# Optimization experiments

Measured on AMD Instinct MI355X. Metric: run time of the kernel, lower is better.

## Reference

```python
import jax, jax.numpy as jnp
import numpy as np

B, S, I, H, O = 64, 1024, 512, 1024, 512

def setup_inputs() -> dict:
    key = jax.random.key(0)
    ks = jax.random.split(key, 4)
    scale_ih = float(np.sqrt(6.0 / (I + H)))
    scale_hh = float(np.sqrt(6.0 / (H + H)))
    scale_ho = float(np.sqrt(6.0 / (H + O)))
    return {
        "inputs": jax.random.normal(ks[0], (B, S, I), dtype=jnp.float32),
        "initial_hidden": jnp.zeros((B, H), dtype=jnp.float32),
        "W_ih": jax.random.uniform(ks[1], (H, I), jnp.float32, -scale_ih, scale_ih),
        "b_ih": jnp.zeros((H,), jnp.float32),
        "W_hh": jax.random.uniform(ks[2], (H, H), jnp.float32, -scale_hh, scale_hh),
        "b_hh": jnp.zeros((H,), jnp.float32),
        "W_ho": jax.random.uniform(ks[3], (O, H), jnp.float32, -scale_ho, scale_ho),
        "b_ho": jnp.zeros((O,), jnp.float32),
    }

def reference(inputs, initial_hidden, W_ih, b_ih, W_hh, b_hh, W_ho, b_ho):
    # h_t = tanh(W_ih x_t + b_ih + W_hh h_{t-1} + b_hh); y_t = W_ho h_t + b_ho
    # Precompute the input projection for all timesteps in one batched GEMM.
    x_proj = jnp.einsum("bsi,hi->bsh", inputs, W_ih) + b_ih + b_hh  # (B,S,H)

    def step(h, xp_t):
        h_new = jnp.tanh(xp_t + h @ W_hh.T)  # (B,H)
        return h_new, h_new

    # scan over time: move seq axis to front
    last_hidden, hs = jax.lax.scan(step, initial_hidden, jnp.swapaxes(x_proj, 0, 1))
    hs = jnp.swapaxes(hs, 0, 1)  # (B,S,H)
    outputs = jnp.einsum("bsh,oh->bso", hs, W_ho) + b_ho  # (B,S,O)
    return outputs, last_hidden
```

## Files before the change

### kernel.cpp

```cpp
#include <hip/hip_runtime.h>
#include <cmath>

#define B_ 64
#define S_ 1024
#define I_ 512
#define H_ 1024
#define O_ 512
#define HB (H_ * B_)
#define SCAN_NBLK 64
#define PROD_NBLK 96
#define WORK_NBLK 96
#define NTHR 512
#define NPROD_PER_S 8
#define SPIN_BUDGET (1 << 22)

typedef __attribute__((ext_vector_type(8))) __bf16 bf16x8;
typedef __attribute__((ext_vector_type(4))) float f32x4;
typedef unsigned long long u64;

__device__ __forceinline__ int fragIdx(int k, int b) {
  int kt = k >> 5, q = (k >> 3) & 3, slot = k & 7;
  int nt = b >> 4, ln = q * 16 + (b & 15);
  return (((kt * 4 + nt) * 64) + ln) * 8 + slot;
}

__device__ __forceinline__ float aload_f32(const float* p) {
  unsigned v = __hip_atomic_load((const unsigned*)p, __ATOMIC_RELAXED,
                                 __HIP_MEMORY_SCOPE_AGENT);
  return __builtin_bit_cast(float, v);
}

__global__ void k_hfrag0(const float* __restrict__ h0,
                         unsigned short* __restrict__ hh,
                         unsigned short* __restrict__ hl) {
  int idx = blockIdx.x * 256 + threadIdx.x;
  int b = idx >> 10, k = idx & 1023;
  float v = h0[(size_t)b * H_ + k];
  __bf16 h = (__bf16)v;
  __bf16 l = (__bf16)(v - (float)h);
  int fi = fragIdx(k, b);
  hh[fi] = __builtin_bit_cast(unsigned short, h);
  hl[fi] = __builtin_bit_cast(unsigned short, l);
}

__global__ __launch_bounds__(NTHR) void k_fused(
    const float* __restrict__ Whh, float* __restrict__ xp,
    unsigned short* __restrict__ hh0, unsigned short* __restrict__ hl0,
    unsigned short* __restrict__ hh1, unsigned short* __restrict__ hl1,
    unsigned* __restrict__ bar,
    const float* __restrict__ Who, const float* __restrict__ bho,
    float* __restrict__ out,
    const float* __restrict__ x, const float* __restrict__ Wih,
    const float* __restrict__ bih, const float* __restrict__ bhh) {
  __shared__ float sh[9216];
  const int t = threadIdx.x;
  unsigned* dn    = bar + 128;
  unsigned* incnt = bar + 256;
  int budget = SPIN_BUDGET;

  if (blockIdx.x < SCAN_NBLK) {
    float* red  = sh;
    float* hbuf = sh + 8192;
    const int lane = t & 63;
    const int w    = t >> 6;
    const int j0   = blockIdx.x * 16;
    const int m    = lane & 15, q = lane >> 4;

    bf16x8 Ahi[4], Alo[4];
    #pragma unroll
    for (int kta = 0; kta < 4; kta++) {
      const float* src = Whh + (size_t)(j0 + m) * H_ + (w * 128 + kta * 32 + q * 8);
      float4 v0 = *(const float4*)src;
      float4 v1 = *(const float4*)(src + 4);
      float vv[8] = {v0.x, v0.y, v0.z, v0.w, v1.x, v1.y, v1.z, v1.w};
      #pragma unroll
      for (int j = 0; j < 8; j++) {
        __bf16 h = (__bf16)vv[j];
        __bf16 l = (__bf16)(vv[j] - (float)h);
        Ahi[kta][j] = h;
        Alo[kta][j] = l;
      }
    }

    const int jA = t >> 6, bA = t & 63;
    const size_t xi0 = (size_t)(j0 + jA) * 64 + bA;
    const size_t xi1 = (size_t)(j0 + 8 + jA) * 64 + bA;

    while (__hip_atomic_load(&incnt[0], __ATOMIC_RELAXED,
                             __HIP_MEMORY_SCOPE_AGENT) < NPROD_PER_S) {
      if (--budget < 0) break;
      __builtin_amdgcn_s_sleep(16);
    }
    float xc0 = aload_f32(&xp[xi0]);
    float xc1 = aload_f32(&xp[xi1]);

    const unsigned short* rdh = hh0;
    const unsigned short* rdl = hl0;
    unsigned short* wrh = hh1;
    unsigned short* wrl = hl1;

    for (int s = 0; s < S_; s++) {
      f32x4 acc0 = 0.f, acc1 = 0.f, acc2 = 0.f, acc3 = 0.f;
      #pragma unroll
      for (int kta = 0; kta < 4; kta++) {
        const int ktg = w * 4 + kta;
        const unsigned short* ph = rdh + ((size_t)(ktg * 4) * 64 + lane) * 8;
        const unsigned short* pl = rdl + ((size_t)(ktg * 4) * 64 + lane) * 8;
        bf16x8 bh0 = __builtin_bit_cast(bf16x8, *(const uint4*)(ph + 0 * 512));
        bf16x8 bh1 = __builtin_bit_cast(bf16x8, *(const uint4*)(ph + 1 * 512));
        bf16x8 bh2 = __builtin_bit_cast(bf16x8, *(const uint4*)(ph + 2 * 512));
        bf16x8 bh3 = __builtin_bit_cast(bf16x8, *(const uint4*)(ph + 3 * 512));
        bf16x8 bl0 = __builtin_bit_cast(bf16x8, *(const uint4*)(pl + 0 * 512));
        bf16x8 bl1 = __builtin_bit_cast(bf16x8, *(const uint4*)(pl + 1 * 512));
        bf16x8 bl2 = __builtin_bit_cast(bf16x8, *(const uint4*)(pl + 2 * 512));
        bf16x8 bl3 = __builtin_bit_cast(bf16x8, *(const uint4*)(pl + 3 * 512));
        acc0 = __builtin_amdgcn_mfma_f32_16x16x32_bf16(Ahi[kta], bh0, acc0, 0, 0, 0);
        acc1 = __builtin_amdgcn_mfma_f32_16x16x32_bf16(Ahi[kta], bh1, acc1, 0, 0, 0);
        acc2 = __builtin_amdgcn_mfma_f32_16x16x32_bf16(Ahi[kta], bh2, acc2, 0, 0, 0);
        acc3 = __builtin_amdgcn_mfma_f32_16x16x32_bf16(Ahi[kta], bh3, acc3, 0, 0, 0);
        acc0 = __builtin_amdgcn_mfma_f32_16x16x32_bf16(Alo[kta], bh0, acc0, 0, 0, 0);
        acc1 = __builtin_amdgcn_mfma_f32_16x16x32_bf16(Alo[kta], bh1, acc1, 0, 0, 0);
        acc2 = __builtin_amdgcn_mfma_f32_16x16x32_bf16(Alo[kta], bh2, acc2, 0, 0, 0);
        acc3 = __builtin_amdgcn_mfma_f32_16x16x32_bf16(Alo[kta], bh3, acc3, 0, 0, 0);
        acc0 = __builtin_amdgcn_mfma_f32_16x16x32_bf16(Ahi[kta], bl0, acc0, 0, 0, 0);
        acc1 = __builtin_amdgcn_mfma_f32_16x16x32_bf16(Ahi[kta], bl1, acc1, 0, 0, 0);
        acc2 = __builtin_amdgcn_mfma_f32_16x16x32_bf16(Ahi[kta], bl2, acc2, 0, 0, 0);
        acc3 = __builtin_amdgcn_mfma_f32_16x16x32_bf16(Ahi[kta], bl3, acc3, 0, 0, 0);
      }
      *(f32x4*)&red[(((w * 4 + 0) * 64) + lane) * 4] = acc0;
      *(f32x4*)&red[(((w * 4 + 1) * 64) + lane) * 4] = acc1;
      *(f32x4*)&red[(((w * 4 + 2) * 64) + lane) * 4] = acc2;
      *(f32x4*)&red[(((w * 4 + 3) * 64) + lane) * 4] = acc3;
      __syncthreads();
      float* hcur = xp + (size_t)s * HB;
      #pragma unroll
      for (int rep = 0; rep < 2; rep++) {
        const int j = jA + rep * 8, b = bA;
        const int nt = b >> 4, lc = (j >> 2) * 16 + (b & 15), reg = j & 3;
        float sum = 0.f;
        #pragma unroll
        for (int ww = 0; ww < 8; ww++)
          sum += red[(((ww * 4 + nt) * 64) + lc) * 4 + reg];
        const size_t xi = (rep == 0) ? xi0 : xi1;
        const float xv = (rep == 0) ? xc0 : xc1;
        float v = tanhf(xv + sum);
        __hip_atomic_store(&hcur[xi], v, __ATOMIC_RELAXED, __HIP_MEMORY_SCOPE_AGENT);
        hbuf[j * 64 + b] = v;
      }
      __syncthreads();
      if (t < 128) {
        const int jg = t >> 6, b = t & 63;
        const int k0 = j0 + jg * 8;
        const int kt = k0 >> 5, qq = (k0 >> 3) & 3;
        const int nt = b >> 4, ln = qq * 16 + (b & 15);
        const size_t fb = ((size_t)((kt * 4 + nt) * 64 + ln)) * 8;
        unsigned hu[8], lu[8];
        #pragma unroll
        for (int jj = 0; jj < 8; jj++) {
          float v = hbuf[(jg * 8 + jj) * 64 + b];
          __bf16 hh = (__bf16)v;
          __bf16 ll = (__bf16)(v - (float)hh);
          hu[jj] = (unsigned)__builtin_bit_cast(unsigned short, hh);
          lu[jj] = (unsigned)__builtin_bit_cast(unsigned short, ll);
        }
        u64 hw0 = (u64)hu[0] | ((u64)hu[1] << 16) | ((u64)hu[2] << 32) | ((u64)hu[3] << 48);
        u64 hw1 = (u64)hu[4] | ((u64)hu[5] << 16) | ((u64)hu[6] << 32) | ((u64)hu[7] << 48);
        u64 lw0 = (u64)lu[0] | ((u64)lu[1] << 16) | ((u64)lu[2] << 32) | ((u64)lu[3] << 48);
        u64 lw1 = (u64)lu[4] | ((u64)lu[5] << 16) | ((u64)lu[6] << 32) | ((u64)lu[7] << 48);
        __hip_atomic_store((u64*)(wrh + fb) + 0, hw0, __ATOMIC_RELAXED, __HIP_MEMORY_SCOPE_AGENT);
        __hip_atomic_store((u64*)(wrh + fb) + 1, hw1, __ATOMIC_RELAXED, __HIP_MEMORY_SCOPE_AGENT);
        __hip_atomic_store((u64*)(wrl + fb) + 0, lw0, __ATOMIC_RELAXED, __HIP_MEMORY_SCOPE_AGENT);
        __hip_atomic_store((u64*)(wrl + fb) + 1, lw1, __ATOMIC_RELAXED, __HIP_MEMORY_SCOPE_AGENT);
      }
      __syncthreads();
      if (t == 0)
        __hip_atomic_store(&bar[blockIdx.x], (unsigned)(s + 1),
                           __ATOMIC_RELAXED, __HIP_MEMORY_SCOPE_AGENT);
      const int sn = s + 1;
      const float* xpn = xp + (size_t)sn * HB;
      if (t >= 64) {
        if (sn < S_) {
          while (__hip_atomic_load(&incnt[sn], __ATOMIC_RELAXED,
                                   __HIP_MEMORY_SCOPE_AGENT) < NPROD_PER_S) {
            if (--budget < 0) break;
            __builtin_amdgcn_s_sleep(1);
          }
          xc0 = aload_f32(&xpn[xi0]); xc1 = aload_f32(&xpn[xi1]);
        }
      } else {
        __builtin_amdgcn_fence(__ATOMIC_ACQUIRE, "agent");
        if (sn < S_) {
          while (__hip_atomic_load(&incnt[sn], __ATOMIC_RELAXED,
                                   __HIP_MEMORY_SCOPE_AGENT) < NPROD_PER_S) {
            if (--budget < 0) break;
            __builtin_amdgcn_s_sleep(1);
          }
          xc0 = aload_f32(&xpn[xi0]); xc1 = aload_f32(&xpn[xi1]);
        }
        const unsigned need = (unsigned)sn;
        while (__hip_atomic_load(&bar[lane], __ATOMIC_RELAXED,
                                 __HIP_MEMORY_SCOPE_AGENT) < need) {
          if (--budget < 0) break;
          __builtin_amdgcn_s_sleep(1);
        }
        if (t == 0 && blockIdx.x == 0)
          __hip_atomic_store(dn, (unsigned)sn,
                             __ATOMIC_RELAXED, __HIP_MEMORY_SCOPE_AGENT);
      }
      __syncthreads();
      const unsigned short* th = rdh; rdh = wrh; wrh = (unsigned short*)th;
      const unsigned short* tl = rdl; rdl = wrl; wrl = (unsigned short*)tl;
    }
  } else if (blockIdx.x < SCAN_NBLK + PROD_NBLK) {
    float* As = sh;
    float* Bs = sh + 128 * 36;
    const int pid = blockIdx.x - SCAN_NBLK;
    const int tx = t & 15, ty = t >> 4;
    const int bS = t >> 3, c4S = (t & 7) * 4;
    for (int item = pid; item < S_ * 8; item += PROD_NBLK) {
      const int s = item >> 3, h00 = (item & 7) << 7;
      float acc[4][4] = {};
      for (int k0 = 0; k0 < I_; k0 += 32) {
        #pragma unroll
        for (int L = 0; L < 2; L++) {
          int f = L * 512 + t;
          int row = f >> 3, c4 = (f & 7) * 4;
          float4 v = *(const float4*)&Wih[(size_t)(h00 + row) * I_ + k0 + c4];
          *(float4*)&As[row * 36 + c4] = v;
        }
        {
          float4 v = *(const float4*)&x[(size_t)bS * (S_ * I_) + (size_t)s * I_ + k0 + c4S];
          Bs[(c4S + 0) * 72 + bS] = v.x;
          Bs[(c4S + 1) * 72 + bS] = v.y;
          Bs[(c4S + 2) * 72 + bS] = v.z;
          Bs[(c4S + 3) * 72 + bS] = v.w;
        }
        __syncthreads();
        #pragma unroll
        for (int k = 0; k < 32; k += 4) {
          float4 a[4], bq[4];
          #pragma unroll
          for (int r = 0; r < 4; r++) a[r] = *(const float4*)&As[(ty * 4 + r) * 36 + k];
          #pragma unroll
          for (int kk = 0; kk < 4; kk++) bq[kk] = *(const float4*)&Bs[(k + kk) * 72 + tx * 4];
          #pragma unroll
          for (int kk = 0; kk < 4; kk++)
            #pragma unroll
            for (int r = 0; r < 4; r++)
              #pragma unroll
              for (int c = 0; c < 4; c++)
                acc[r][c] += ((const float*)&a[r])[kk] * ((const float*)&bq[kk])[c];
        }
        __syncthreads();
      }
      #pragma unroll
      for (int r = 0; r < 4; r++) {
        const int h = h00 + ty * 4 + r;
        const float bias = bih[h] + bhh[h];
        float2 p0 = {acc[r][0] + bias, acc[r][1] + bias};
        float2 p1 = {acc[r][2] + bias, acc[r][3] + bias};
        u64* dst = (u64*)&xp[(size_t)s * HB + (size_t)h * 64 + tx * 4];
        __hip_atomic_store(dst + 0, __builtin_bit_cast(u64, p0),
                           __ATOMIC_RELAXED, __HIP_MEMORY_SCOPE_AGENT);
        __hip_atomic_store(dst + 1, __builtin_bit_cast(u64, p1),
                           __ATOMIC_RELAXED, __HIP_MEMORY_SCOPE_AGENT);
      }
      __syncthreads();
      if (t == 0)
        __hip_atomic_fetch_add(&incnt[s], 1u,
                               __ATOMIC_RELAXED, __HIP_MEMORY_SCOPE_AGENT);
    }
  } else {
    float* As = sh;
    float* Bs = sh + 32 * 68;
    const int wid = blockIdx.x - SCAN_NBLK - PROD_NBLK;
    const int tx = t & 31, ty = t >> 5;
    const int kkA = t >> 4, b4 = (t & 15) * 4;
    for (int item = wid; item < S_ * 4; item += WORK_NBLK) {
      const int s = item >> 2, o0 = (item & 3) << 7;
      if (t == 0) {
        const unsigned need = (unsigned)(s + 1);
        while (__hip_atomic_load(dn, __ATOMIC_RELAXED,
                                 __HIP_MEMORY_SCOPE_AGENT) < need) {
          if (--budget < 0) break;
          __builtin_amdgcn_s_sleep(8);
        }
      }
      __syncthreads();
      const float* hsS = xp + (size_t)s * HB;
      float acc[4][4] = {};
      for (int k0 = 0; k0 < H_; k0 += 32) {
        const u64* hp = (const u64*)&hsS[(size_t)(k0 + kkA) * 64 + b4];
        u64 w0 = __hip_atomic_load(hp + 0, __ATOMIC_RELAXED, __HIP_MEMORY_SCOPE_AGENT);
        u64 w1 = __hip_atomic_load(hp + 1, __ATOMIC_RELAXED, __HIP_MEMORY_SCOPE_AGENT);
        *(float2*)&As[kkA * 68 + b4 + 0] = __builtin_bit_cast(float2, w0);
        *(float2*)&As[kkA * 68 + b4 + 2] = __builtin_bit_cast(float2, w1);
        #pragma unroll
        for (int L = 0; L < 2; L++) {
          int f = L * 512 + t;
          int row = f >> 3, c4 = (f & 7) * 4;
          float4 v = *(const float4*)&Who[(size_t)(o0 + row) * H_ + k0 + c4];
          Bs[(c4 + 0) * 132 + row] = v.x;
          Bs[(c4 + 1) * 132 + row] = v.y;
          Bs[(c4 + 2) * 132 + row] = v.z;
          Bs[(c4 + 3) * 132 + row] = v.w;
        }
        __syncthreads();
        #pragma unroll
        for (int k = 0; k < 32; k++) {
          float4 a4 = *(const float4*)&As[k * 68 + ty * 4];
          float4 bq = *(const float4*)&Bs[k * 132 + tx * 4];
          #pragma unroll
          for (int r = 0; r < 4; r++)
            #pragma unroll
            for (int c = 0; c < 4; c++)
              acc[r][c] += ((const float*)&a4)[r] * ((const float*)&bq)[c];
        }
        __syncthreads();
      }
      #pragma unroll
      for (int r = 0; r < 4; r++) {
        const int b = ty * 4 + r;
        float4 o4;
        o4.x = acc[r][0] + bho[o0 + tx * 4 + 0];
        o4.y = acc[r][1] + bho[o0 + tx * 4 + 1];
        o4.z = acc[r][2] + bho[o0 + tx * 4 + 2];
        o4.w = acc[r][3] + bho[o0 + tx * 4 + 3];
        *(float4*)&out[(size_t)b * (S_ * O_) + (size_t)s * O_ + o0 + tx * 4] = o4;
      }
    }
  }
}

__global__ void k_lasth(const float* __restrict__ hlast, float* __restrict__ out) {
  int idx = blockIdx.x * 256 + threadIdx.x;
  int b = idx >> 10, h = idx & 1023;
  out[idx] = hlast[h * 64 + b];
}

extern "C" void kernel_launch(void* const* d_in, const int* in_sizes, int n_in,
                              void* d_out, int out_size, void* d_ws, size_t ws_size,
                              hipStream_t stream) {
  const float* x    = (const float*)d_in[0];
  const float* h0   = (const float*)d_in[1];
  const float* Wih  = (const float*)d_in[2];
  const float* bih  = (const float*)d_in[3];
  const float* Whh  = (const float*)d_in[4];
  const float* bhh  = (const float*)d_in[5];
  const float* Who  = (const float*)d_in[6];
  const float* bho  = (const float*)d_in[7];
  float* out = (float*)d_out;

  float* xp = (float*)d_ws;
  unsigned short* hh0 = (unsigned short*)(xp + (size_t)S_ * HB);
  unsigned short* hl0 = hh0 + HB;
  unsigned short* hh1 = hl0 + HB;
  unsigned short* hl1 = hh1 + HB;
  unsigned* bar = (unsigned*)(hl1 + HB);

  hipMemsetAsync(bar, 0, 8192, stream);
  k_hfrag0<<<256, 256, 0, stream>>>(h0, hh0, hl0);

  void* args[] = {(void*)&Whh, (void*)&xp, (void*)&hh0, (void*)&hl0,
                  (void*)&hh1, (void*)&hl1, (void*)&bar,
                  (void*)&Who, (void*)&bho, (void*)&out,
                  (void*)&x, (void*)&Wih, (void*)&bih, (void*)&bhh};
  hipLaunchCooperativeKernel((const void*)k_fused,
                             dim3(SCAN_NBLK + PROD_NBLK + WORK_NBLK), dim3(NTHR),
                             args, 0, stream);

  k_lasth<<<256, 256, 0, stream>>>(xp + (size_t)(S_ - 1) * HB, out + (size_t)B_ * S_ * O_);
}
```

Measured before the change: 6.426 ms.

## Halve scan blocks to 32, each computing 32 hidden rows, and add producer blocks

Each recurrent-scan block now owns 32 rows of W_hh (two 16-row MFMA tiles) rather than 16. That halves the number of blocks in the per-step grid barrier, and the freed CUs go to the input-projection producer and output worker roles. The xp prefetch now uses plain loads after a compiler memory barrier instead of atomic loads, and the spin budget and sleep interval are reduced. The risks are double the MFMA work per block on the serial critical path, extra register pressure from twice as many A fragments, and correctness that depends on plain loads seeing values other blocks just wrote.

New measurement: 6.196 ms. -3.6%, faster.

```diff
diff --git a/kernel.cpp b/kernel.cpp
--- a/kernel.cpp
+++ b/kernel.cpp
@@ -7,12 +7,12 @@
 #define H_ 1024
 #define O_ 512
 #define HB (H_ * B_)
-#define SCAN_NBLK 64
-#define PROD_NBLK 96
-#define WORK_NBLK 96
+#define SCAN_NBLK 32
+#define PROD_NBLK 112
+#define WORK_NBLK 112
 #define NTHR 512
 #define NPROD_PER_S 8
-#define SPIN_BUDGET (1 << 22)
+#define SPIN_BUDGET (1 << 20)
 
 typedef __attribute__((ext_vector_type(8))) __bf16 bf16x8;
 typedef __attribute__((ext_vector_type(4))) float f32x4;
@@ -22,12 +22,6 @@
   int kt = k >> 5, q = (k >> 3) & 3, slot = k & 7;
   int nt = b >> 4, ln = q * 16 + (b & 15);
   return (((kt * 4 + nt) * 64) + ln) * 8 + slot;
-}
-
-__device__ __forceinline__ float aload_f32(const float* p) {
-  unsigned v = __hip_atomic_load((const unsigned*)p, __ATOMIC_RELAXED,
-                                 __HIP_MEMORY_SCOPE_AGENT);
-  return __builtin_bit_cast(float, v);
 }
 
 __global__ void k_hfrag0(const float* __restrict__ h0,
@@ -52,7 +46,7 @@
     float* __restrict__ out,
     const float* __restrict__ x, const float* __restrict__ Wih,
     const float* __restrict__ bih, const float* __restrict__ bhh) {
-  __shared__ float sh[9216];
+  __shared__ float sh[10240];
   const int t = threadIdx.x;
   unsigned* dn    = bar + 128;
   unsigned* incnt = bar + 256;
@@ -63,36 +57,45 @@
     float* hbuf = sh + 8192;
     const int lane = t & 63;
     const int w    = t >> 6;
-    const int j0   = blockIdx.x * 16;
+    const int j0   = blockIdx.x * 32;
     const int m    = lane & 15, q = lane >> 4;
 
-    bf16x8 Ahi[4], Alo[4];
+    bf16x8 Ahi[2][4], Alo[2][4];
     #pragma unroll
-    for (int kta = 0; kta < 4; kta++) {
-      const float* src = Whh + (size_t)(j0 + m) * H_ + (w * 128 + kta * 32 + q * 8);
-      float4 v0 = *(const float4*)src;
-      float4 v1 = *(const float4*)(src + 4);
-      float vv[8] = {v0.x, v0.y, v0.z, v0.w, v1.x, v1.y, v1.z, v1.w};
-      #pragma unroll
-      for (int j = 0; j < 8; j++) {
-        __bf16 h = (__bf16)vv[j];
-        __bf16 l = (__bf16)(vv[j] - (float)h);
-        Ahi[kta][j] = h;
-        Alo[kta][j] = l;
-      }
-    }
+    for (int mt = 0; mt < 2; mt++)
+      #pragma unroll
+      for (int kta = 0; kta < 4; kta++) {
+        const float* src = Whh + (size_t)(j0 + mt * 16 + m) * H_ +
+                           (w * 128 + kta * 32 + q * 8);
+        float4 v0 = *(const float4*)src;
+        float4 v1 = *(const float4*)(src + 4);
+        float vv[8] = {v0.x, v0.y, v0.z, v0.w, v1.x, v1.y, v1.z, v1.w};
+        #pragma unroll
+        for (int j = 0; j < 8; j++) {
+          __bf16 h = (__bf16)vv[j];
+          __bf16 l = (__bf16)(vv[j] - (float)h);
+          Ahi[mt][kta][j] = h;
+          Alo[mt][kta][j] = l;
+        }
+      }
 
     const int jA = t >> 6, bA = t & 63;
-    const size_t xi0 = (size_t)(j0 + jA) * 64 + bA;
-    const size_t xi1 = (size_t)(j0 + 8 + jA) * 64 + bA;
+    size_t xia[4];
+    #pragma unroll
+    for (int mt = 0; mt < 2; mt++)
+      #pragma unroll
+      for (int rep = 0; rep < 2; rep++)
+        xia[mt * 2 + rep] = (size_t)(j0 + mt * 16 + jA + rep * 8) * 64 + bA;
 
     while (__hip_atomic_load(&incnt[0], __ATOMIC_RELAXED,
                              __HIP_MEMORY_SCOPE_AGENT) < NPROD_PER_S) {
       if (--budget < 0) break;
-      __builtin_amdgcn_s_sleep(16);
+      __builtin_amdgcn_s_sleep(8);
     }
-    float xc0 = aload_f32(&xp[xi0]);
-    float xc1 = aload_f32(&xp[xi1]);
+    asm volatile("" ::: "memory");
+    float xc[4];
+    #pragma unroll
+    for (int p = 0; p < 4; p++) xc[p] = xp[xia[p]];
 
     const unsigned short* rdh = hh0;
     const unsigned short* rdl = hl0;
@@ -100,7 +103,11 @@
     unsigned short* wrl = hl1;
 
     for (int s = 0; s < S_; s++) {
-      f32x4 acc0 = 0.f, acc1 = 0.f, acc2 = 0.f, acc3 = 0.f;
+      f32x4 acc[2][4];
+      #pragma unroll
+      for (int mt = 0; mt < 2; mt++)
+        #pragma unroll
+        for (int i = 0; i < 4; i++) acc[mt][i] = 0.f;
       #pragma unroll
       for (int kta = 0; kta < 4; kta++) {
         const int ktg = w * 4 + kta;
@@ -114,41 +121,45 @@
         bf16x8 bl1 = __builtin_bit_cast(bf16x8, *(const uint4*)(pl + 1 * 512));
         bf16x8 bl2 = __builtin_bit_cast(bf16x8, *(const uint4*)(pl + 2 * 512));
         bf16x8 bl3 = __builtin_bit_cast(bf16x8, *(const uint4*)(pl + 3 * 512));
-        acc0 = __builtin_amdgcn_mfma_f32_16x16x32_bf16(Ahi[kta], bh0, acc0, 0, 0, 0);
-        acc1 = __builtin_amdgcn_mfma_f32_16x16x32_bf16(Ahi[kta], bh1, acc1, 0, 0, 0);
-        acc2 = __builtin_amdgcn_mfma_f32_16x16x32_bf16(Ahi[kta], bh2, acc2, 0, 0, 0);
-        acc3 = __builtin_amdgcn_mfma_f32_16x16x32_bf16(Ahi[kta], bh3, acc3, 0, 0, 0);
-        acc0 = __builtin_amdgcn_mfma_f32_16x16x32_bf16(Alo[kta], bh0, acc0, 0, 0, 0);
-        acc1 = __builtin_amdgcn_mfma_f32_16x16x32_bf16(Alo[kta], bh1, acc1, 0, 0, 0);
-        acc2 = __builtin_amdgcn_mfma_f32_16x16x32_bf16(Alo[kta], bh2, acc2, 0, 0, 0);
-        acc3 = __builtin_amdgcn_mfma_f32_16x16x32_bf16(Alo[kta], bh3, acc3, 0, 0, 0);
-        acc0 = __builtin_amdgcn_mfma_f32_16x16x32_bf16(Ahi[kta], bl0, acc0, 0, 0, 0);
-        acc1 = __builtin_amdgcn_mfma_f32_16x16x32_bf16(Ahi[kta], bl1, acc1, 0, 0, 0);
-        acc2 = __builtin_amdgcn_mfma_f32_16x16x32_bf16(Ahi[kta], bl2, acc2, 0, 0, 0);
-        acc3 = __builtin_amdgcn_mfma_f32_16x16x32_bf16(Ahi[kta], bl3, acc3, 0, 0, 0);
-      }
-      *(f32x4*)&red[(((w * 4 + 0) * 64) + lane) * 4] = acc0;
-      *(f32x4*)&red[(((w * 4 + 1) * 64) + lane) * 4] = acc1;
-      *(f32x4*)&red[(((w * 4 + 2) * 64) + lane) * 4] = acc2;
-      *(f32x4*)&red[(((w * 4 + 3) * 64) + lane) * 4] = acc3;
-      __syncthreads();
+        #pragma unroll
+        for (int mt = 0; mt < 2; mt++) {
+          acc[mt][0] = __builtin_amdgcn_mfma_f32_16x16x32_bf16(Ahi[mt][kta], bh0, acc[mt][0], 0, 0, 0);
+          acc[mt][1] = __builtin_amdgcn_mfma_f32_16x16x32_bf16(Ahi[mt][kta], bh1, acc[mt][1], 0, 0, 0);
+          acc[mt][2] = __builtin_amdgcn_mfma_f32_16x16x32_bf16(Ahi[mt][kta], bh2, acc[mt][2], 0, 0, 0);
+          acc[mt][3] = __builtin_amdgcn_mfma_f32_16x16x32_bf16(Ahi[mt][kta], bh3, acc[mt][3], 0, 0, 0);
+          acc[mt][0] = __builtin_amdgcn_mfma_f32_16x16x32_bf16(Alo[mt][kta], bh0, acc[mt][0], 0, 0, 0);
+          acc[mt][1] = __builtin_amdgcn_mfma_f32_16x16x32_bf16(Alo[mt][kta], bh1, acc[mt][1], 0, 0, 0);
+          acc[mt][2] = __builtin_amdgcn_mfma_f32_16x16x32_bf16(Alo[mt][kta], bh2, acc[mt][2], 0, 0, 0);
+          acc[mt][3] = __builtin_amdgcn_mfma_f32_16x16x32_bf16(Alo[mt][kta], bh3, acc[mt][3], 0, 0, 0);
+          acc[mt][0] = __builtin_amdgcn_mfma_f32_16x16x32_bf16(Ahi[mt][kta], bl0, acc[mt][0], 0, 0, 0);
+          acc[mt][1] = __builtin_amdgcn_mfma_f32_16x16x32_bf16(Ahi[mt][kta], bl1, acc[mt][1], 0, 0, 0);
+          acc[mt][2] = __builtin_amdgcn_mfma_f32_16x16x32_bf16(Ahi[mt][kta], bl2, acc[mt][2], 0, 0, 0);
+          acc[mt][3] = __builtin_amdgcn_mfma_f32_16x16x32_bf16(Ahi[mt][kta], bl3, acc[mt][3], 0, 0, 0);
+        }
+      }
       float* hcur = xp + (size_t)s * HB;
       #pragma unroll
-      for (int rep = 0; rep < 2; rep++) {
-        const int j = jA + rep * 8, b = bA;
-        const int nt = b >> 4, lc = (j >> 2) * 16 + (b & 15), reg = j & 3;
-        float sum = 0.f;
-        #pragma unroll
-        for (int ww = 0; ww < 8; ww++)
-          sum += red[(((ww * 4 + nt) * 64) + lc) * 4 + reg];
-        const size_t xi = (rep == 0) ? xi0 : xi1;
-        const float xv = (rep == 0) ? xc0 : xc1;
-        float v = tanhf(xv + sum);
-        __hip_atomic_store(&hcur[xi], v, __ATOMIC_RELAXED, __HIP_MEMORY_SCOPE_AGENT);
-        hbuf[j * 64 + b] = v;
-      }
-      __syncthreads();
-      if (t < 128) {
+      for (int mt = 0; mt < 2; mt++) {
+        #pragma unroll
+        for (int i = 0; i < 4; i++)
+          *(f32x4*)&red[(((w * 4 + i) * 64) + lane) * 4] = acc[mt][i];
+        __syncthreads();
+        #pragma unroll
+        for (int rep = 0; rep < 2; rep++) {
+          const int j = jA + rep * 8, b = bA;
+          const int nt = b >> 4, lc = (j >> 2) * 16 + (b & 15), reg = j & 3;
+          float sum = 0.f;
+          #pragma unroll
+          for (int ww = 0; ww < 8; ww++)
+            sum += red[(((ww * 4 + nt) * 64) + lc) * 4 + reg];
+          float v = tanhf(xc[mt * 2 + rep] + sum);
+          __hip_atomic_store(&hcur[xia[mt * 2 + rep]], v,
+                             __ATOMIC_RELAXED, __HIP_MEMORY_SCOPE_AGENT);
+          hbuf[(mt * 16 + j) * 64 + b] = v;
+        }
+        __syncthreads();
+      }
+      if (t < 256) {
         const int jg = t >> 6, b = t & 63;
         const int k0 = j0 + jg * 8;
         const int kt = k0 >> 5, qq = (k0 >> 3) & 3;
@@ -185,7 +196,9 @@
             if (--budget < 0) break;
             __builtin_amdgcn_s_sleep(1);
           }
-          xc0 = aload_f32(&xpn[xi0]); xc1 = aload_f32(&xpn[xi1]);
+          asm volatile("" ::: "memory");
+          #pragma unroll
+          for (int p = 0; p < 4; p++) xc[p] = xpn[xia[p]];
         }
       } else {
         __builtin_amdgcn_fence(__ATOMIC_ACQUIRE, "agent");
@@ -195,13 +208,17 @@
             if (--budget < 0) break;
             __builtin_amdgcn_s_sleep(1);
           }
-          xc0 = aload_f32(&xpn[xi0]); xc1 = aload_f32(&xpn[xi1]);
-        }
-        const unsigned need = (unsigned)sn;
-        while (__hip_atomic_load(&bar[lane], __ATOMIC_RELAXED,
-                                 __HIP_MEMORY_SCOPE_AGENT) < need) {
-          if (--budget < 0) break;
-          __builtin_amdgcn_s_sleep(1);
+          asm volatile("" ::: "memory");
+          #pragma unroll
+          for (int p = 0; p < 4; p++) xc[p] = xpn[xia[p]];
+        }
+        if (lane < SCAN_NBLK) {
+          const unsigned need = (unsigned)sn;
+          while (__hip_atomic_load(&bar[lane], __ATOMIC_RELAXED,
+                                   __HIP_MEMORY_SCOPE_AGENT) < need) {
+            if (--budget < 0) break;
+            __builtin_amdgcn_s_sleep(1);
+          }
         }
         if (t == 0 && blockIdx.x == 0)
           __hip_atomic_store(dn, (unsigned)sn,
```
